# Performance work log

Hardware: AMD Instinct MI355X
Metric: run time of the kernel (lower is better)

## Reference

```python
import jax, jax.numpy as jnp
import numpy as np
from jax import lax

N_EXPERTS = 8
TOP_K_EXPERTS = 2
N_PRIMITIVES = 16
TOP_K_PRIM = 4
RANK = 64
D_MODEL = 512
D_FF = 2048
BATCH, SEQ = 8, 2048
TEMPERATURE = 1.0
EPS = 1e-8


def setup_inputs() -> dict:
    key = jax.random.key(0)
    ks = jax.random.split(key, 8)
    x = jax.random.normal(ks[0], (BATCH, SEQ, D_MODEL), dtype=jnp.float32)
    Wr = jax.random.normal(ks[1], (N_EXPERTS, D_MODEL), dtype=jnp.float32) * 0.02
    fc1_logits = jax.random.normal(ks[2], (N_EXPERTS, N_PRIMITIVES), dtype=jnp.float32)
    fc2_logits = jax.random.normal(ks[3], (N_EXPERTS, N_PRIMITIVES), dtype=jnp.float32)
    A1 = jax.random.normal(ks[4], (N_PRIMITIVES, D_MODEL, RANK), dtype=jnp.float32) * 0.02
    B1 = jax.random.normal(ks[5], (N_PRIMITIVES, RANK, D_FF), dtype=jnp.float32) * 0.02
    A2 = jax.random.normal(ks[6], (N_PRIMITIVES, D_FF, RANK), dtype=jnp.float32) * 0.02
    B2 = jax.random.normal(ks[7], (N_PRIMITIVES, RANK, D_MODEL), dtype=jnp.float32) * 0.02
    return {"x": x, "Wr": Wr, "fc1_logits": fc1_logits, "fc2_logits": fc2_logits,
            "A1": A1, "B1": B1, "A2": A2, "B2": B2}


def _compose_fused(logits, A, B):
    """Build per-expert fused low-rank maps from primitive bank.
    logits: (E, P); A: (P, d_in, r); B: (P, r, d_out).
    Returns A_cat (E, d_in, k*r), B_cat (E, k*r, d_out)."""
    w = jax.nn.softmax(logits / TEMPERATURE, axis=-1)            # (E, P)
    top_w, top_idx = lax.top_k(w, TOP_K_PRIM)                     # (E, k)
    top_w = top_w / (top_w.sum(axis=-1, keepdims=True) + EPS)
    sqrt_w = jnp.sqrt(top_w + EPS)                                # (E, k)
    A_sel = A[top_idx] * sqrt_w[:, :, None, None]                 # (E, k, d_in, r)
    B_sel = B[top_idx] * sqrt_w[:, :, None, None]                 # (E, k, r, d_out)
    E = logits.shape[0]
    A_cat = jnp.transpose(A_sel, (0, 2, 1, 3)).reshape(E, A.shape[1], TOP_K_PRIM * RANK)
    B_cat = B_sel.reshape(E, TOP_K_PRIM * RANK, B.shape[2])
    return A_cat, B_cat


def reference(x, Wr, fc1_logits, fc2_logits, A1, B1, A2, B2):
    Bsz, S, D = x.shape
    T = Bsz * S
    xt = x.reshape(T, D)

    # --- router: top-k expert selection ---
    router_logits = xt @ Wr.T                                     # (T, E)
    router_probs = jax.nn.softmax(router_logits, axis=-1)         # (T, E)
    top_w, top_idx = lax.top_k(router_probs, TOP_K_EXPERTS)       # (T, K)
    top_w = top_w / (top_w.sum(axis=-1, keepdims=True) + EPS)
    rows = jnp.arange(T)[:, None]
    gate = jnp.zeros((T, N_EXPERTS), x.dtype).at[rows, top_idx].add(top_w)
    expert_mask = jnp.zeros((T, N_EXPERTS), x.dtype).at[rows, top_idx].set(1.0)

    # --- load balancing aux loss (Switch Transformer) ---
    tokens_per_expert = expert_mask.sum(axis=0)
    f = tokens_per_expert / (tokens_per_expert.sum() + EPS)
    P = router_probs.mean(axis=0)
    aux_loss = N_EXPERTS * jnp.sum(f * P)

    # --- per-expert composed FFN over shared primitive banks ---
    A1c, B1c = _compose_fused(fc1_logits, A1, B1)                 # (E, D, kr), (E, kr, Dff)
    A2c, B2c = _compose_fused(fc2_logits, A2, B2)                 # (E, Dff, kr), (E, kr, D)

    out = jnp.zeros((T, D), x.dtype)
    for e in range(N_EXPERTS):  # small fixed expert loop keeps peak memory at one expert's d_ff activation
        h = jax.nn.gelu((xt @ A1c[e]) @ B1c[e], approximate=False)  # (T, Dff)
        y = (h @ A2c[e]) @ B2c[e]                                   # (T, D)
        out = out + gate[:, e:e + 1] * y

    return out.reshape(Bsz, S, D), aux_loss
```

## Files before the change

kernel.cpp:

```cpp
#include <hip/hip_runtime.h>

#define T_TOK 16384
#define DM    512
#define DFF   2048
#define NE    8
#define NP    16
#define KP    4
#define RANK  64
#define KR    256
#define EPSF  1e-8f
#define CAP   6144
#define MT_E  48

typedef unsigned short u16;
typedef __bf16 bf16x8 __attribute__((ext_vector_type(8)));
typedef float  f32x4  __attribute__((ext_vector_type(4)));
typedef unsigned short u16x8v __attribute__((ext_vector_type(8)));
typedef unsigned short u16x4v __attribute__((ext_vector_type(4)));

typedef __attribute__((address_space(3))) void as3_void;
typedef __attribute__((address_space(1))) void as1_void;

__device__ __forceinline__ u16 f2bf(float f) {
  return __builtin_bit_cast(u16, (__bf16)f);
}
__device__ __forceinline__ float bf2f(u16 v) {
  unsigned int u = ((unsigned int)v) << 16;
  return __builtin_bit_cast(float, u);
}

__device__ __forceinline__ void gl_lds16(const u16* g, u16* l) {
  __builtin_amdgcn_global_load_lds((as1_void*)g, (as3_void*)l, 16, 0, 0);
}


__device__ __forceinline__ void stage_tile(const u16* g, int ld, u16* lds_tile, int tid) {
  int row = tid >> 3, cc = tid & 7;
#pragma unroll
  for (int ri = 0; ri < 4; ri++) {
    int rg = ri * 32 + row;
    gl_lds16(g + (size_t)rg * ld + ((cc ^ (rg & 7)) * 8), &lds_tile[rg * 64 + cc * 8]);
  }
}

__global__ void zero_kernel(int* __restrict__ cnt, float* __restrict__ probsum) {
  int i = blockIdx.x * 256 + threadIdx.x;
  if (i < NE) cnt[i] = 0;
  if (i >= NE && i < NE + NE * 64) probsum[i - NE] = 0.f;
}

__global__ void compose_meta(const float* __restrict__ fc1, const float* __restrict__ fc2,
                             float* __restrict__ sw1, int* __restrict__ idx1,
                             float* __restrict__ sw2, int* __restrict__ idx2) {
  int tid = threadIdx.x;
  if (tid >= 16) return;
  const float* src = (tid < 8) ? fc1 : fc2;
  float* sw = (tid < 8) ? sw1 : sw2;
  int*  idx = (tid < 8) ? idx1 : idx2;
  int e = tid & 7;
  float wv[NP];
  float mx = -1e30f;
  for (int p = 0; p < NP; p++) { wv[p] = src[e * NP + p]; mx = fmaxf(mx, wv[p]); }
  float sum = 0.f;
  for (int p = 0; p < NP; p++) { wv[p] = __expf(wv[p] - mx); sum += wv[p]; }
  float inv = 1.f / sum;
  for (int p = 0; p < NP; p++) wv[p] *= inv;
  float tw[KP]; int ti[KP];
  for (int k = 0; k < KP; k++) {
    int best = 0; float bv = -1.f;
    for (int p = 0; p < NP; p++) if (wv[p] > bv) { bv = wv[p]; best = p; }
    tw[k] = bv; ti[k] = best; wv[best] = -2.f;
  }
  float ts = tw[0] + tw[1] + tw[2] + tw[3];
  float invt = 1.f / (ts + EPSF);
  for (int k = 0; k < KP; k++) {
    sw[e * KP + k] = sqrtf(tw[k] * invt + EPSF);
    idx[e * KP + k] = ti[k];
  }
}

__global__ __launch_bounds__(256) void build_W1p(
    const float* __restrict__ A1, const int* __restrict__ idx1,
    const float* __restrict__ sw1, u16* __restrict__ W1p) {
  __shared__ u16 Ta[2 * 64 * 68];
  int bid = blockIdx.x;
  int k0i = bid & 7, ntile = (bid >> 3) & 1, e = bid >> 4;
  int d0 = k0i * 64;
  int tid = threadIdx.x;
  {
    int kk = tid >> 7, row = (tid >> 1) & 63, half = tid & 1;
    int prim = idx1[e * 4 + ntile * 2 + kk];
    float s = sw1[e * 4 + ntile * 2 + kk];
#pragma unroll
    for (int q = 0; q < 8; q++) {
      int r = half * 32 + q * 4;
      float4 v = *(const float4*)(A1 + ((size_t)prim * DM + d0 + row) * RANK + r);
      u16x4v o;
      o[0] = f2bf(v.x * s); o[1] = f2bf(v.y * s);
      o[2] = f2bf(v.z * s); o[3] = f2bf(v.w * s);
      *(u16x4v*)&Ta[(kk * 64 + row) * 68 + r] = o;
    }
  }
  __syncthreads();
  u16* dst = W1p + ((size_t)(e * 2 + ntile) * 8 + k0i) * 8192;
#pragma unroll
  for (int it = 0; it < 4; it++) {
    int slot = it * 256 + tid;
    int lane = slot & 63, rest = slot >> 6;
    int nt = rest & 3, ks = (rest >> 2) & 1, wn = rest >> 3;
    int ln = lane & 15, quad = lane >> 4;
    int r = nt * 16 + ln;
    int db = ks * 32 + quad * 8;
    u16x8v o;
#pragma unroll
    for (int j = 0; j < 8; j++) o[j] = Ta[(wn * 64 + db + j) * 68 + r];
    *(u16x8v*)&dst[((wn * 8 + ks * 4 + nt) * 64 + lane) * 8] = o;
  }
}

__global__ __launch_bounds__(256) void build_V1p(
    const float* __restrict__ B1, const int* __restrict__ idx1,
    const float* __restrict__ sw1, u16* __restrict__ V1p) {
  __shared__ u16 Tb[64 * 132];
  int bid = blockIdx.x;
  int p = bid & 3, f0i = (bid >> 2) & 15, e = bid >> 6;
  int prim = idx1[e * 4 + p];
  float s = sw1[e * 4 + p];
  int f0 = f0i * 128;
  int tid = threadIdx.x;
  {
    int r = tid >> 2, fq = (tid & 3) * 32;
#pragma unroll
    for (int q = 0; q < 8; q++) {
      int fl = fq + q * 4;
      float4 v = *(const float4*)(B1 + ((size_t)prim * RANK + r) * DFF + f0 + fl);
      u16x4v o;
      o[0] = f2bf(v.x * s); o[1] = f2bf(v.y * s);
      o[2] = f2bf(v.z * s); o[3] = f2bf(v.w * s);
      *(u16x4v*)&Tb[r * 132 + fl] = o;
    }
  }
  __syncthreads();
  u16* dst = V1p + ((size_t)e << 19) + f0i * 32768 + p * 8192;
#pragma unroll
  for (int it = 0; it < 4; it++) {
    int slot = it * 256 + tid;
    int lane = slot & 63, nt = (slot >> 6) & 1, ks = (slot >> 7) & 1, wv = slot >> 8;
    int ln = lane & 15, quad = lane >> 4;
    int fl = wv * 32 + nt * 16 + ln;
    int r0 = ks * 32 + quad * 8;
    u16x8v o;
#pragma unroll
    for (int j = 0; j < 8; j++) o[j] = Tb[(r0 + j) * 132 + fl];
    *(u16x8v*)&dst[(((wv * 2 + ks) * 2 + nt) * 64 + lane) * 8] = o;
  }
}

__global__ __launch_bounds__(256) void build_W2p(
    const float* __restrict__ A2, const int* __restrict__ idx2,
    const float* __restrict__ sw2, u16* __restrict__ W2p) {
  __shared__ u16 Ta[2 * 64 * 68];
  int bid = blockIdx.x;
  int c2 = bid & 3, f0i = (bid >> 2) & 15, e = bid >> 6;
  int hh = c2 >> 1, fi = c2 & 1;
  int f0 = f0i * 128 + fi * 64;
  int tid = threadIdx.x;
  {
    int kk = tid >> 7, row = (tid >> 1) & 63, half = tid & 1;
    int prim = idx2[e * 4 + hh * 2 + kk];
    float s = sw2[e * 4 + hh * 2 + kk];
#pragma unroll
    for (int q = 0; q < 8; q++) {
      int r = half * 32 + q * 4;
      float4 v = *(const float4*)(A2 + ((size_t)prim * DFF + f0 + row) * RANK + r);
      u16x4v o;
      o[0] = f2bf(v.x * s); o[1] = f2bf(v.y * s);
      o[2] = f2bf(v.z * s); o[3] = f2bf(v.w * s);
      *(u16x4v*)&Ta[(kk * 64 + row) * 68 + r] = o;
    }
  }
  __syncthreads();
  u16* dst = W2p + ((size_t)e << 19) + f0i * 32768 + c2 * 8192;
#pragma unroll
  for (int it = 0; it < 4; it++) {
    int slot = it * 256 + tid;
    int lane = slot & 63, nt = (slot >> 6) & 1, ks = (slot >> 7) & 1, wv = slot >> 8;
    int ln = lane & 15, quad = lane >> 4;
    int kk = wv >> 1;
    int r = (wv & 1) * 32 + nt * 16 + ln;
    int fb = ks * 32 + quad * 8;
    u16x8v o;
#pragma unroll
    for (int j = 0; j < 8; j++) o[j] = Ta[(kk * 64 + fb + j) * 68 + r];
    *(u16x8v*)&dst[(((wv * 2 + ks) * 2 + nt) * 64 + lane) * 8] = o;
  }
}

__global__ __launch_bounds__(256) void build_V2p(
    const float* __restrict__ B2, const int* __restrict__ idx2,
    const float* __restrict__ sw2, u16* __restrict__ V2p) {
  __shared__ u16 Tb[64 * 132];
  int bid = blockIdx.x;
  int k0i = bid & 3, ntile = (bid >> 2) & 3, e = bid >> 4;
  int prim = idx2[e * 4 + k0i];
  float s = sw2[e * 4 + k0i];
  int tid = threadIdx.x;
  {
    int r = tid >> 2, dq = (tid & 3) * 32;
#pragma unroll
    for (int q = 0; q < 8; q++) {
      int dd = dq + q * 4;
      float4 v = *(const float4*)(B2 + ((size_t)prim * RANK + r) * DM + ntile * 128 + dd);
      u16x4v o;
      o[0] = f2bf(v.x * s); o[1] = f2bf(v.y * s);
      o[2] = f2bf(v.z * s); o[3] = f2bf(v.w * s);
      *(u16x4v*)&Tb[r * 132 + dd] = o;
    }
  }
  __syncthreads();
  u16* dst = V2p + ((size_t)(e * 4 + ntile) * 4 + k0i) * 8192;
#pragma unroll
  for (int it = 0; it < 4; it++) {
    int slot = it * 256 + tid;
    int lane = slot & 63, rest = slot >> 6;
    int nt = rest & 3, ks = (rest >> 2) & 1, wn = rest >> 3;
    int ln = lane & 15, quad = lane >> 4;
    int dd = wn * 64 + nt * 16 + ln;
    int r0 = ks * 32 + quad * 8;
    u16x8v o;
#pragma unroll
    for (int j = 0; j < 8; j++) o[j] = Tb[(r0 + j) * 132 + dd];
    *(u16x8v*)&dst[((wn * 8 + ks * 4 + nt) * 64 + lane) * 8] = o;
  }
}

__global__ __launch_bounds__(256) void router_kernel(
    const float* __restrict__ x, const float* __restrict__ Wr,
    float* __restrict__ probsum, int* __restrict__ eidx,
    float* __restrict__ gate) {
  __shared__ float wr_s[NE * 4 * 132];
  __shared__ float ps_s[NE];
  int tid = threadIdx.x;
  if (tid < NE) ps_s[tid] = 0.f;
  for (int i = tid; i < NE * DM; i += 256) {
    int e = i >> 9, k = i & 511;
    wr_s[(e * 4 + (k >> 7)) * 132 + (k & 127)] = Wr[i];
  }
  __syncthreads();
  int lane = tid & 63, wv = tid >> 6;
  int tl = lane & 15, sl = lane >> 4;
  int t = blockIdx.x * 64 + wv * 16 + tl;
  const float* xp = x + (size_t)t * DM + sl * 128;
  const float* wp = &wr_s[sl * 132];
  float acc[NE];
#pragma unroll
  for (int e = 0; e < NE; e++) acc[e] = 0.f;
  for (int c = 0; c < 32; c++) {
    float4 xv = *(const float4*)(xp + c * 4);
#pragma unroll
    for (int e = 0; e < NE; e++) {
      float4 w4 = *(const float4*)(wp + e * 4 * 132 + c * 4);
      acc[e] += xv.x * w4.x + xv.y * w4.y + xv.z * w4.z + xv.w * w4.w;
    }
  }
#pragma unroll
  for (int e = 0; e < NE; e++) {
    acc[e] += __shfl_xor(acc[e], 16, 64);
    acc[e] += __shfl_xor(acc[e], 32, 64);
  }
  if (sl == 0) {
    float mx = acc[0];
#pragma unroll
    for (int e = 1; e < NE; e++) mx = fmaxf(mx, acc[e]);
    float pe[NE]; float sum = 0.f;
#pragma unroll
    for (int e = 0; e < NE; e++) { pe[e] = __expf(acc[e] - mx); sum += pe[e]; }
    float inv = 1.f / sum;
#pragma unroll
    for (int e = 0; e < NE; e++) pe[e] *= inv;
    int i0 = 0;
#pragma unroll
    for (int e = 1; e < NE; e++) if (pe[e] > pe[i0]) i0 = e;
    int i1 = (i0 == 0) ? 1 : 0;
#pragma unroll
    for (int e = 0; e < NE; e++) if (e != i0 && pe[e] > pe[i1]) i1 = e;
    float p0 = pe[i0], p1 = pe[i1];
    float gd = 1.f / (p0 + p1 + EPSF);
    eidx[t] = i0 | (i1 << 3);
    gate[i0 * T_TOK + t] = p0 * gd;
    gate[i1 * T_TOK + t] = p1 * gd;
#pragma unroll
    for (int e = 0; e < NE; e++) atomicAdd(&ps_s[e], pe[e]);
  }
  __syncthreads();
  if (tid < NE) atomicAdd(&probsum[tid * 64 + (blockIdx.x & 63)], ps_s[tid]);
}

__global__ void scatter_kernel(const int* __restrict__ eidx,
                               int* __restrict__ cnt, int* __restrict__ perm,
                               int* __restrict__ slots) {
  __shared__ int hist[NE], base[NE];
  int tid = threadIdx.x;
  if (tid < NE) hist[tid] = 0;
  __syncthreads();
  int t = blockIdx.x * 256 + tid;
  int pk = eidx[t];
  int e0 = pk & 7, e1 = (pk >> 3) & 7;
  int p0 = atomicAdd(&hist[e0], 1);
  int p1 = atomicAdd(&hist[e1], 1);
  __syncthreads();
  if (tid < NE) base[tid] = atomicAdd(&cnt[tid], hist[tid]);
  __syncthreads();
  int g0 = base[e0] + p0; if (g0 >= CAP) g0 = CAP - 1;
  int g1 = base[e1] + p1; if (g1 >= CAP) g1 = CAP - 1;
  perm[e0 * T_TOK + g0] = t;
  perm[e1 * T_TOK + g1] = t;
  slots[t * 2]     = e0 * CAP + g0;
  slots[t * 2 + 1] = e1 * CAP + g1;
}

__global__ void aux_kernel(const int* __restrict__ cnt, const float* __restrict__ probsum,
                           float* __restrict__ aux_out) {
  int lane = threadIdx.x;
  if (lane >= 64) return;
  float s[NE];
#pragma unroll
  for (int e = 0; e < NE; e++) {
    float v = probsum[e * 64 + lane];
#pragma unroll
    for (int off = 32; off > 0; off >>= 1) v += __shfl_xor(v, off, 64);
    s[e] = v;
  }
  if (lane == 0) {
    float c[NE]; float cs = 0.f;
    for (int e = 0; e < NE; e++) { c[e] = (float)cnt[e]; cs += c[e]; }
    float aux = 0.f;
    for (int e = 0; e < NE; e++)
      aux += (c[e] / (cs + EPSF)) * (s[e] / (float)T_TOK);
    *aux_out = (float)NE * aux;
  }
}


__global__ __launch_bounds__(256) void k1_u(
    const float* __restrict__ x, const int* __restrict__ cnt,
    const int* __restrict__ perm, const u16* __restrict__ W1p,
    u16* __restrict__ u) {
  __shared__ __align__(16) u16 As[8192];
  __shared__ int tok_s[128];
  int bid = blockIdx.x;
  int e = bid & 7;
  int r0 = bid >> 3;
  int ntile = r0 & 1, mt = r0 >> 1;
  int m0 = mt << 7;
  int cntE = cnt[e];
  if (m0 >= cntE) return;
  int tid = threadIdx.x;
  if (tid < 128) {
    int mm = m0 + tid; if (mm > cntE - 1) mm = cntE - 1;
    tok_s[tid] = perm[e * T_TOK + mm];
  }
  __syncthreads();
  int wv = tid >> 6, lane = tid & 63;
  int wm = wv >> 1, wn = wv & 1, ln = lane & 15, quad = lane >> 4;
  int sw = (ln & 7) << 3;
  const u16* Wbase = W1p + ((size_t)(e * 2 + ntile) * 8) * 8192 + (wn * 8 * 64 + lane) * 8;
  int kst = mt & 7;
  f32x4 acc[4][4];
#pragma unroll
  for (int a = 0; a < 4; a++)
#pragma unroll
    for (int b = 0; b < 4; b++) acc[a][b] = (f32x4){0.f, 0.f, 0.f, 0.f};
  for (int kk = 0; kk < 8; kk++) {
    int k0i = (kk + kst) & 7;
    bf16x8 bf[2][4];
    const u16* Wf = Wbase + (size_t)k0i * 8192;
#pragma unroll
    for (int ks = 0; ks < 2; ks++)
#pragma unroll
      for (int nt = 0; nt < 4; nt++)
        bf[ks][nt] = *(const bf16x8*)&Wf[(ks * 4 + nt) * 512];
    for (int i = tid; i < 2048; i += 256) {
      int row = i >> 4, c4 = i & 15;
      float4 v = *(const float4*)(x + (size_t)tok_s[row] * DM + k0i * 64 + c4 * 4);
      u16x4v o; o[0] = f2bf(v.x); o[1] = f2bf(v.y); o[2] = f2bf(v.z); o[3] = f2bf(v.w);
      *(u16x4v*)&As[row * 64 + ((c4 * 4) ^ ((row & 7) << 3))] = o;
    }
    __syncthreads();
#pragma unroll
    for (int ks = 0; ks < 2; ks++) {
      bf16x8 af[4];
      int co = (ks * 32 + quad * 8) ^ sw;
#pragma unroll
      for (int mt2 = 0; mt2 < 4; mt2++)
        af[mt2] = *(const bf16x8*)&As[(wm * 64 + mt2 * 16 + ln) * 64 + co];
      __builtin_amdgcn_s_setprio(1);
#pragma unroll
      for (int mt2 = 0; mt2 < 4; mt2++)
#pragma unroll
        for (int nt = 0; nt < 4; nt++)
          acc[mt2][nt] = __builtin_amdgcn_mfma_f32_16x16x32_bf16(af[mt2], bf[ks][nt], acc[mt2][nt], 0, 0, 0);
      __builtin_amdgcn_s_setprio(0);
    }
    __syncthreads();
  }
  int slot0 = e * CAP + m0;
#pragma unroll
  for (int mt2 = 0; mt2 < 4; mt2++)
#pragma unroll
    for (int nt = 0; nt < 4; nt++)
#pragma unroll
      for (int r = 0; r < 4; r++) {
        int row = wm * 64 + mt2 * 16 + quad * 4 + r;
        int col = ntile * 128 + wn * 64 + nt * 16 + ln;
        u[(size_t)(slot0 + row) * KR + col] = f2bf(acc[mt2][nt][r]);
      }
}

__global__ __launch_bounds__(256, 2) void k23(
    const u16* __restrict__ u, const int* __restrict__ cnt,
    const u16* __restrict__ V1p, const u16* __restrict__ W2p,
    u16* __restrict__ t) {
  __shared__ __align__(16) u16 Us16[64 * 128];
  __shared__ __align__(16) u16 Hs[64 * 128];
  int bid = blockIdx.x;
  int e = bid & 7, mt = bid >> 3;
  int m0 = mt << 6;
  int cntE = cnt[e];
  if (m0 >= cntE) return;
  int tid = threadIdx.x;
  int slot0 = e * CAP + m0;
  const u16* ub = u + (size_t)slot0 * KR;

#pragma unroll
  for (int r = 0; r < 4; r++) {
    int i = r * 256 + tid;
    int row = i >> 4, cc = i & 15;
    gl_lds16(ub + (size_t)row * 256 + 128 + ((cc ^ (row & 7)) * 8), &Us16[i * 8]);
  }

  int wv = tid >> 6, lane = tid & 63;
  int ln = lane & 15, quad = lane >> 4;
  int sw = (ln & 7) << 3;

  bf16x8 ureg[2][2][4];
#pragma unroll
  for (int p = 0; p < 2; p++)
#pragma unroll
    for (int ks = 0; ks < 2; ks++)
#pragma unroll
      for (int m = 0; m < 4; m++)
        ureg[p][ks][m] = *(const bf16x8*)&ub[(size_t)(m * 16 + ln) * KR + p * 64 + ks * 32 + quad * 8];

  __syncthreads();

  const u16* V1w = V1p + ((size_t)e << 19) + wv * 2048 + lane * 8;
  const u16* W2w = W2p + ((size_t)e << 19) + wv * 2048 + lane * 8;

  f32x4 tacc[4][4];
#pragma unroll
  for (int a = 0; a < 4; a++)
#pragma unroll
    for (int b = 0; b < 4; b++) tacc[a][b] = (f32x4){0.f, 0.f, 0.f, 0.f};
  f32x4 hacc[4][2];

  int fst = mt & 15;
  for (int ii = 0; ii < 16; ii++) {
    int f0i = (ii + fst) & 15;
    const u16* V1f = V1w + f0i * 32768;
    const u16* W2f = W2w + f0i * 32768;
#pragma unroll
    for (int p = 0; p < 4; p++) {
      bf16x8 bf[2][2];
#pragma unroll
      for (int ks = 0; ks < 2; ks++)
#pragma unroll
        for (int nt = 0; nt < 2; nt++)
          bf[ks][nt] = *(const bf16x8*)&V1f[p * 8192 + (ks * 2 + nt) * 512];
      if (p == 0) {
#pragma unroll
        for (int a = 0; a < 4; a++)
#pragma unroll
          for (int b = 0; b < 2; b++) hacc[a][b] = (f32x4){0.f, 0.f, 0.f, 0.f};
      }
      if (p < 2) {
        __builtin_amdgcn_s_setprio(1);
#pragma unroll
        for (int ks = 0; ks < 2; ks++)
#pragma unroll
          for (int m = 0; m < 4; m++)
#pragma unroll
            for (int nt = 0; nt < 2; nt++)
              hacc[m][nt] = __builtin_amdgcn_mfma_f32_16x16x32_bf16(ureg[p][ks][m], bf[ks][nt], hacc[m][nt], 0, 0, 0);
        __builtin_amdgcn_s_setprio(0);
      } else {
        bf16x8 af[2][4];
#pragma unroll
        for (int ks = 0; ks < 2; ks++) {
          int cu = ((p - 2) * 64 + ks * 32 + quad * 8) ^ sw;
#pragma unroll
          for (int m = 0; m < 4; m++)
            af[ks][m] = *(const bf16x8*)&Us16[((m * 16 + ln) << 7) + cu];
        }
        __builtin_amdgcn_s_setprio(1);
#pragma unroll
        for (int ks = 0; ks < 2; ks++)
#pragma unroll
          for (int m = 0; m < 4; m++)
#pragma unroll
            for (int nt = 0; nt < 2; nt++)
              hacc[m][nt] = __builtin_amdgcn_mfma_f32_16x16x32_bf16(af[ks][m], bf[ks][nt], hacc[m][nt], 0, 0, 0);
        __builtin_amdgcn_s_setprio(0);
      }
    }
    __syncthreads();
#pragma unroll
    for (int m = 0; m < 4; m++)
#pragma unroll
      for (int nt = 0; nt < 2; nt++)
#pragma unroll
        for (int r = 0; r < 4; r++) {
          int row = m * 16 + quad * 4 + r;
          int col = wv * 32 + nt * 16 + ln;
          float v = hacc[m][nt][r];
          float s = 1.f / (1.f + __expf(-1.702f * v));
          Hs[(row << 7) + (col ^ ((row & 7) << 3))] = f2bf(v * s);
        }
    __syncthreads();
#pragma unroll
    for (int c2 = 0; c2 < 4; c2++) {
      const int hh = c2 >> 1, fi = c2 & 1;
      bf16x8 bf[2][2], af[2][4];
#pragma unroll
      for (int ks = 0; ks < 2; ks++)
#pragma unroll
        for (int nt = 0; nt < 2; nt++)
          bf[ks][nt] = *(const bf16x8*)&W2f[c2 * 8192 + (ks * 2 + nt) * 512];
#pragma unroll
      for (int ks = 0; ks < 2; ks++) {
        int ch = (fi * 64 + ks * 32 + quad * 8) ^ sw;
#pragma unroll
        for (int m = 0; m < 4; m++)
          af[ks][m] = *(const bf16x8*)&Hs[((m * 16 + ln) << 7) + ch];
      }
      __builtin_amdgcn_s_setprio(1);
#pragma unroll
      for (int ks = 0; ks < 2; ks++)
#pragma unroll
        for (int m = 0; m < 4; m++)
#pragma unroll
          for (int nt = 0; nt < 2; nt++)
            tacc[m][hh * 2 + nt] = __builtin_amdgcn_mfma_f32_16x16x32_bf16(af[ks][m], bf[ks][nt], tacc[m][hh * 2 + nt], 0, 0, 0);
      __builtin_amdgcn_s_setprio(0);
    }
  }
#pragma unroll
  for (int m = 0; m < 4; m++)
#pragma unroll
    for (int hh = 0; hh < 2; hh++)
#pragma unroll
      for (int nt = 0; nt < 2; nt++)
#pragma unroll
        for (int r = 0; r < 4; r++) {
          int row = m * 16 + quad * 4 + r;
          int col = hh * 128 + wv * 32 + nt * 16 + ln;
          t[(size_t)(slot0 + row) * KR + col] = f2bf(tacc[m][hh * 2 + nt][r]);
        }
}

__global__ __launch_bounds__(256) void k4_y(
    const u16* __restrict__ t, const int* __restrict__ cnt,
    const int* __restrict__ perm, const float* __restrict__ gate,
    const u16* __restrict__ V2p, u16* __restrict__ y) {
  __shared__ __align__(16) u16 As[8192];
  __shared__ float g_s[128];
  int bid = blockIdx.x;
  int e = bid & 7;
  int r0 = bid >> 3;
  int ntile = r0 & 3, mt = r0 >> 2;
  int m0 = mt << 7;
  int cntE = cnt[e];
  if (m0 >= cntE) return;
  int tid = threadIdx.x;
  if (tid < 128) {
    int mm = m0 + tid; if (mm > cntE - 1) mm = cntE - 1;
    int tk = perm[e * T_TOK + mm];
    g_s[tid] = gate[e * T_TOK + tk];
  }
  __syncthreads();
  int slot0 = e * CAP + m0;
  const u16* Abase = t + (size_t)slot0 * KR;
  int wv = tid >> 6, lane = tid & 63;
  int wm = wv >> 1, wn = wv & 1, ln = lane & 15, quad = lane >> 4;
  int sw = (ln & 7) << 3;
  const u16* Wbase = V2p + ((size_t)(e * 4 + ntile) * 4) * 8192 + (wn * 8 * 64 + lane) * 8;
  int kst = mt & 3;
  f32x4 acc[4][4];
#pragma unroll
  for (int a = 0; a < 4; a++)
#pragma unroll
    for (int b = 0; b < 4; b++) acc[a][b] = (f32x4){0.f, 0.f, 0.f, 0.f};
  for (int kk = 0; kk < 4; kk++) {
    int k0i = (kk + kst) & 3;
    bf16x8 bf[2][4];
    const u16* Wf = Wbase + (size_t)k0i * 8192;
#pragma unroll
    for (int ks = 0; ks < 2; ks++)
#pragma unroll
      for (int nt = 0; nt < 4; nt++)
        bf[ks][nt] = *(const bf16x8*)&Wf[(ks * 4 + nt) * 512];
    stage_tile(Abase + k0i * 64, KR, As, tid);
    __syncthreads();
#pragma unroll
    for (int ks = 0; ks < 2; ks++) {
      bf16x8 af[4];
      int co = (ks * 32 + quad * 8) ^ sw;
#pragma unroll
      for (int mt2 = 0; mt2 < 4; mt2++)
        af[mt2] = *(const bf16x8*)&As[(wm * 64 + mt2 * 16 + ln) * 64 + co];
      __builtin_amdgcn_s_setprio(1);
#pragma unroll
      for (int mt2 = 0; mt2 < 4; mt2++)
#pragma unroll
        for (int nt = 0; nt < 4; nt++)
          acc[mt2][nt] = __builtin_amdgcn_mfma_f32_16x16x32_bf16(af[mt2], bf[ks][nt], acc[mt2][nt], 0, 0, 0);
      __builtin_amdgcn_s_setprio(0);
    }
    __syncthreads();
  }
#pragma unroll
  for (int mt2 = 0; mt2 < 4; mt2++)
#pragma unroll
    for (int nt = 0; nt < 4; nt++)
#pragma unroll
      for (int r = 0; r < 4; r++) {
        int row = wm * 64 + mt2 * 16 + quad * 4 + r;
        int col = ntile * 128 + wn * 64 + nt * 16 + ln;
        y[(size_t)(slot0 + row) * DM + col] = f2bf(acc[mt2][nt][r] * g_s[row]);
      }
}

__global__ void gather_kernel(const u16* __restrict__ y, const int* __restrict__ slots,
                              float* __restrict__ out) {
  int idx = blockIdx.x * 256 + threadIdx.x;
  int t = idx >> 7, c4 = (idx & 127) * 4;
  int sA = slots[t * 2], sB = slots[t * 2 + 1];
  u16x4v a = *(const u16x4v*)&y[(size_t)sA * DM + c4];
  u16x4v b = *(const u16x4v*)&y[(size_t)sB * DM + c4];
  float4 o;
  o.x = bf2f(a[0]) + bf2f(b[0]);
  o.y = bf2f(a[1]) + bf2f(b[1]);
  o.z = bf2f(a[2]) + bf2f(b[2]);
  o.w = bf2f(a[3]) + bf2f(b[3]);
  *(float4*)&out[(size_t)t * DM + c4] = o;
}

extern "C" void kernel_launch(void* const* d_in, const int* in_sizes, int n_in,
                              void* d_out, int out_size, void* d_ws, size_t ws_size,
                              hipStream_t stream) {
  const float* x   = (const float*)d_in[0];
  const float* Wr  = (const float*)d_in[1];
  const float* fc1 = (const float*)d_in[2];
  const float* fc2 = (const float*)d_in[3];
  const float* A1  = (const float*)d_in[4];
  const float* B1  = (const float*)d_in[5];
  const float* A2  = (const float*)d_in[6];
  const float* B2  = (const float*)d_in[7];
  float* out = (float*)d_out;

  char* ws = (char*)d_ws;
  float* sw1     = (float*)(ws + 0);
  int*   idx1    = (int*)(ws + 512);
  float* sw2     = (float*)(ws + 1024);
  int*   idx2    = (int*)(ws + 1536);
  int*   cnt     = (int*)(ws + 2048);
  float* probsum = (float*)(ws + 2560);
  int*   eidx    = (int*)(ws + 8192);
  int*   slots   = (int*)(ws + 8192 + 65536);
  float* gate    = (float*)(ws + 8192 + 65536 + 131072);
  int*   perm    = (int*)(ws + 8192 + 65536 + 131072 + 524288);
  u16*   W1p     = (u16*)(ws + 8192 + 65536 + 131072 + 2 * 524288);
  u16*   V1p     = W1p + 1048576;
  u16*   W2p     = V1p + 4194304;
  u16*   V2p     = W2p + 4194304;
  char*  endW    = (char*)(V2p + 1048576);
  u16*   u_buf   = (u16*)endW;
  u16*   t_buf   = (u16*)(endW + 25165824);
  u16*   y_buf   = (u16*)(endW + 2 * 25165824);

  zero_kernel<<<3, 256, 0, stream>>>(cnt, probsum);
  compose_meta<<<1, 64, 0, stream>>>(fc1, fc2, sw1, idx1, sw2, idx2);
  build_W1p<<<128, 256, 0, stream>>>(A1, idx1, sw1, W1p);
  build_V1p<<<512, 256, 0, stream>>>(B1, idx1, sw1, V1p);
  build_W2p<<<512, 256, 0, stream>>>(A2, idx2, sw2, W2p);
  build_V2p<<<128, 256, 0, stream>>>(B2, idx2, sw2, V2p);
  router_kernel<<<T_TOK / 64, 256, 0, stream>>>(x, Wr, probsum, eidx, gate);
  scatter_kernel<<<T_TOK / 256, 256, 0, stream>>>(eidx, cnt, perm, slots);
  aux_kernel<<<1, 64, 0, stream>>>(cnt, probsum, out + (out_size - 1));

  k1_u<<<2 * NE * MT_E, 256, 0, stream>>>(x, cnt, perm, W1p, u_buf);
  k23<<<NE * (CAP / 64), 256, 0, stream>>>(u_buf, cnt, V1p, W2p, t_buf);
  k4_y<<<4 * NE * MT_E, 256, 0, stream>>>(t_buf, cnt, perm, gate, V2p, y_buf);
  gather_kernel<<<T_TOK * DM / 4 / 256, 256, 0, stream>>>(y_buf, slots, out);
}
```

Baseline: 340.3 us.

## Double-buffer LDS tiles to drop trailing barriers and stagger start offsets

Shared-memory A tiles in k1_u and k4_y, and the H tile in k23, become ping-pong buffers. This lets each loop iteration drop its trailing __syncthreads, since the next stage writes into the other buffer. Start offsets for the K/F loops are spread with a multiply-by-5 rotation, and in k23 the order of the register and LDS phases plus the two output halves alternates by tile index. The aim is fewer barriers and less contention when blocks hit the same weight slices, at the cost of doubled LDS use, which may lower occupancy, and an unused empty lambda left in the code.

Result: slower. 490.6 us (+44.2%).

```diff
diff --git a/kernel.cpp b/kernel.cpp
--- a/kernel.cpp
+++ b/kernel.cpp
@@ -346,7 +346,7 @@
     const float* __restrict__ x, const int* __restrict__ cnt,
     const int* __restrict__ perm, const u16* __restrict__ W1p,
     u16* __restrict__ u) {
-  __shared__ __align__(16) u16 As[8192];
+  __shared__ __align__(16) u16 As[2][8192];
   __shared__ int tok_s[128];
   int bid = blockIdx.x;
   int e = bid & 7;
@@ -365,7 +365,7 @@
   int wm = wv >> 1, wn = wv & 1, ln = lane & 15, quad = lane >> 4;
   int sw = (ln & 7) << 3;
   const u16* Wbase = W1p + ((size_t)(e * 2 + ntile) * 8) * 8192 + (wn * 8 * 64 + lane) * 8;
-  int kst = mt & 7;
+  int kst = (mt * 5) & 7;
   f32x4 acc[4][4];
 #pragma unroll
   for (int a = 0; a < 4; a++)
@@ -373,6 +373,7 @@
     for (int b = 0; b < 4; b++) acc[a][b] = (f32x4){0.f, 0.f, 0.f, 0.f};
   for (int kk = 0; kk < 8; kk++) {
     int k0i = (kk + kst) & 7;
+    u16* Ac = As[kk & 1];
     bf16x8 bf[2][4];
     const u16* Wf = Wbase + (size_t)k0i * 8192;
 #pragma unroll
@@ -384,7 +385,7 @@
       int row = i >> 4, c4 = i & 15;
       float4 v = *(const float4*)(x + (size_t)tok_s[row] * DM + k0i * 64 + c4 * 4);
       u16x4v o; o[0] = f2bf(v.x); o[1] = f2bf(v.y); o[2] = f2bf(v.z); o[3] = f2bf(v.w);
-      *(u16x4v*)&As[row * 64 + ((c4 * 4) ^ ((row & 7) << 3))] = o;
+      *(u16x4v*)&Ac[row * 64 + ((c4 * 4) ^ ((row & 7) << 3))] = o;
     }
     __syncthreads();
 #pragma unroll
@@ -393,7 +394,7 @@
       int co = (ks * 32 + quad * 8) ^ sw;
 #pragma unroll
       for (int mt2 = 0; mt2 < 4; mt2++)
-        af[mt2] = *(const bf16x8*)&As[(wm * 64 + mt2 * 16 + ln) * 64 + co];
+        af[mt2] = *(const bf16x8*)&Ac[(wm * 64 + mt2 * 16 + ln) * 64 + co];
       __builtin_amdgcn_s_setprio(1);
 #pragma unroll
       for (int mt2 = 0; mt2 < 4; mt2++)
@@ -402,7 +403,6 @@
           acc[mt2][nt] = __builtin_amdgcn_mfma_f32_16x16x32_bf16(af[mt2], bf[ks][nt], acc[mt2][nt], 0, 0, 0);
       __builtin_amdgcn_s_setprio(0);
     }
-    __syncthreads();
   }
   int slot0 = e * CAP + m0;
 #pragma unroll
@@ -422,7 +422,7 @@
     const u16* __restrict__ V1p, const u16* __restrict__ W2p,
     u16* __restrict__ t) {
   __shared__ __align__(16) u16 Us16[64 * 128];
-  __shared__ __align__(16) u16 Hs[64 * 128];
+  __shared__ __align__(16) u16 Hs[2][64 * 128];
   int bid = blockIdx.x;
   int e = bid & 7, mt = bid >> 3;
   int m0 = mt << 6;
@@ -464,56 +464,71 @@
     for (int b = 0; b < 4; b++) tacc[a][b] = (f32x4){0.f, 0.f, 0.f, 0.f};
   f32x4 hacc[4][2];
 
-  int fst = mt & 15;
+  int fst  = (mt * 5) & 15;
+  int arot = (mt >> 4) & 1;
+  int brot = (mt >> 4) & 1;
+
+  auto phA_reg = [&](const u16* V1f) {
+#pragma unroll
+    for (int p = 0; p < 2; p++) {
+      bf16x8 bf[2][2];
+#pragma unroll
+      for (int ks = 0; ks < 2; ks++)
+#pragma unroll
+        for (int nt = 0; nt < 2; nt++)
+          bf[ks][nt] = *(const bf16x8*)&V1f[p * 8192 + (ks * 2 + nt) * 512];
+      __builtin_amdgcn_s_setprio(1);
+#pragma unroll
+      for (int ks = 0; ks < 2; ks++)
+#pragma unroll
+        for (int m = 0; m < 4; m++)
+#pragma unroll
+          for (int nt = 0; nt < 2; nt++)
+            hacc[m][nt] = __builtin_amdgcn_mfma_f32_16x16x32_bf16(ureg[p][ks][m], bf[ks][nt], hacc[m][nt], 0, 0, 0);
+      __builtin_amdgcn_s_setprio(0);
+    }
+  };
+  auto phA_lds = [&](const u16* V1f) {
+#pragma unroll
+    for (int p = 2; p < 4; p++) {
+      bf16x8 bf[2][2], af[2][4];
+#pragma unroll
+      for (int ks = 0; ks < 2; ks++)
+#pragma unroll
+        for (int nt = 0; nt < 2; nt++)
+          bf[ks][nt] = *(const bf16x8*)&V1f[p * 8192 + (ks * 2 + nt) * 512];
+#pragma unroll
+      for (int ks = 0; ks < 2; ks++) {
+        int cu = ((p - 2) * 64 + ks * 32 + quad * 8) ^ sw;
+#pragma unroll
+        for (int m = 0; m < 4; m++)
+          af[ks][m] = *(const bf16x8*)&Us16[((m * 16 + ln) << 7) + cu];
+      }
+      __builtin_amdgcn_s_setprio(1);
+#pragma unroll
+      for (int ks = 0; ks < 2; ks++)
+#pragma unroll
+        for (int m = 0; m < 4; m++)
+#pragma unroll
+          for (int nt = 0; nt < 2; nt++)
+            hacc[m][nt] = __builtin_amdgcn_mfma_f32_16x16x32_bf16(af[ks][m], bf[ks][nt], hacc[m][nt], 0, 0, 0);
+      __builtin_amdgcn_s_setprio(0);
+    }
+  };
+  auto phB = [&](const u16* W2f, const u16* Hc, int hh_c2base) {
+  };
+
   for (int ii = 0; ii < 16; ii++) {
     int f0i = (ii + fst) & 15;
     const u16* V1f = V1w + f0i * 32768;
     const u16* W2f = W2w + f0i * 32768;
-#pragma unroll
-    for (int p = 0; p < 4; p++) {
-      bf16x8 bf[2][2];
-#pragma unroll
-      for (int ks = 0; ks < 2; ks++)
-#pragma unroll
-        for (int nt = 0; nt < 2; nt++)
-          bf[ks][nt] = *(const bf16x8*)&V1f[p * 8192 + (ks * 2 + nt) * 512];
-      if (p == 0) {
-#pragma unroll
-        for (int a = 0; a < 4; a++)
-#pragma unroll
-          for (int b = 0; b < 2; b++) hacc[a][b] = (f32x4){0.f, 0.f, 0.f, 0.f};
-      }
-      if (p < 2) {
-        __builtin_amdgcn_s_setprio(1);
-#pragma unroll
-        for (int ks = 0; ks < 2; ks++)
-#pragma unroll
-          for (int m = 0; m < 4; m++)
-#pragma unroll
-            for (int nt = 0; nt < 2; nt++)
-              hacc[m][nt] = __builtin_amdgcn_mfma_f32_16x16x32_bf16(ureg[p][ks][m], bf[ks][nt], hacc[m][nt], 0, 0, 0);
-        __builtin_amdgcn_s_setprio(0);
-      } else {
-        bf16x8 af[2][4];
-#pragma unroll
-        for (int ks = 0; ks < 2; ks++) {
-          int cu = ((p - 2) * 64 + ks * 32 + quad * 8) ^ sw;
-#pragma unroll
-          for (int m = 0; m < 4; m++)
-            af[ks][m] = *(const bf16x8*)&Us16[((m * 16 + ln) << 7) + cu];
-        }
-        __builtin_amdgcn_s_setprio(1);
-#pragma unroll
-        for (int ks = 0; ks < 2; ks++)
-#pragma unroll
-          for (int m = 0; m < 4; m++)
-#pragma unroll
-            for (int nt = 0; nt < 2; nt++)
-              hacc[m][nt] = __builtin_amdgcn_mfma_f32_16x16x32_bf16(af[ks][m], bf[ks][nt], hacc[m][nt], 0, 0, 0);
-        __builtin_amdgcn_s_setprio(0);
-      }
-    }
-    __syncthreads();
+    u16* Hc = Hs[ii & 1];
+#pragma unroll
+    for (int a = 0; a < 4; a++)
+#pragma unroll
+      for (int b = 0; b < 2; b++) hacc[a][b] = (f32x4){0.f, 0.f, 0.f, 0.f};
+    if (arot) { phA_lds(V1f); phA_reg(V1f); }
+    else      { phA_reg(V1f); phA_lds(V1f); }
 #pragma unroll
     for (int m = 0; m < 4; m++)
 #pragma unroll
@@ -524,36 +539,67 @@
           int col = wv * 32 + nt * 16 + ln;
           float v = hacc[m][nt][r];
           float s = 1.f / (1.f + __expf(-1.702f * v));
-          Hs[(row << 7) + (col ^ ((row & 7) << 3))] = f2bf(v * s);
+          Hc[(row << 7) + (col ^ ((row & 7) << 3))] = f2bf(v * s);
         }
     __syncthreads();
 #pragma unroll
-    for (int c2 = 0; c2 < 4; c2++) {
-      const int hh = c2 >> 1, fi = c2 & 1;
-      bf16x8 bf[2][2], af[2][4];
-#pragma unroll
-      for (int ks = 0; ks < 2; ks++)
-#pragma unroll
-        for (int nt = 0; nt < 2; nt++)
-          bf[ks][nt] = *(const bf16x8*)&W2f[c2 * 8192 + (ks * 2 + nt) * 512];
-#pragma unroll
-      for (int ks = 0; ks < 2; ks++) {
-        int ch = (fi * 64 + ks * 32 + quad * 8) ^ sw;
-#pragma unroll
-        for (int m = 0; m < 4; m++)
-          af[ks][m] = *(const bf16x8*)&Hs[((m * 16 + ln) << 7) + ch];
+    for (int half = 0; half < 2; half++) {
+      if ((half == 0) != (brot != 0)) {
+#pragma unroll
+        for (int fi = 0; fi < 2; fi++) {
+          bf16x8 bf[2][2], af[2][4];
+#pragma unroll
+          for (int ks = 0; ks < 2; ks++)
+#pragma unroll
+            for (int nt = 0; nt < 2; nt++)
+              bf[ks][nt] = *(const bf16x8*)&W2f[(0 * 2 + fi) * 8192 + (ks * 2 + nt) * 512];
+#pragma unroll
+          for (int ks = 0; ks < 2; ks++) {
+            int ch = (fi * 64 + ks * 32 + quad * 8) ^ sw;
+#pragma unroll
+            for (int m = 0; m < 4; m++)
+              af[ks][m] = *(const bf16x8*)&Hc[((m * 16 + ln) << 7) + ch];
+          }
+          __builtin_amdgcn_s_setprio(1);
+#pragma unroll
+          for (int ks = 0; ks < 2; ks++)
+#pragma unroll
+            for (int m = 0; m < 4; m++)
+#pragma unroll
+              for (int nt = 0; nt < 2; nt++)
+                tacc[m][0 * 2 + nt] = __builtin_amdgcn_mfma_f32_16x16x32_bf16(af[ks][m], bf[ks][nt], tacc[m][0 * 2 + nt], 0, 0, 0);
+          __builtin_amdgcn_s_setprio(0);
+        }
+      } else {
+#pragma unroll
+        for (int fi = 0; fi < 2; fi++) {
+          bf16x8 bf[2][2], af[2][4];
+#pragma unroll
+          for (int ks = 0; ks < 2; ks++)
+#pragma unroll
+            for (int nt = 0; nt < 2; nt++)
+              bf[ks][nt] = *(const bf16x8*)&W2f[(1 * 2 + fi) * 8192 + (ks * 2 + nt) * 512];
+#pragma unroll
+          for (int ks = 0; ks < 2; ks++) {
+            int ch = (fi * 64 + ks * 32 + quad * 8) ^ sw;
+#pragma unroll
+            for (int m = 0; m < 4; m++)
+              af[ks][m] = *(const bf16x8*)&Hc[((m * 16 + ln) << 7) + ch];
+          }
+          __builtin_amdgcn_s_setprio(1);
+#pragma unroll
+          for (int ks = 0; ks < 2; ks++)
+#pragma unroll
+            for (int m = 0; m < 4; m++)
+#pragma unroll
+              for (int nt = 0; nt < 2; nt++)
+                tacc[m][1 * 2 + nt] = __builtin_amdgcn_mfma_f32_16x16x32_bf16(af[ks][m], bf[ks][nt], tacc[m][1 * 2 + nt], 0, 0, 0);
+          __builtin_amdgcn_s_setprio(0);
+        }
       }
-      __builtin_amdgcn_s_setprio(1);
-#pragma unroll
-      for (int ks = 0; ks < 2; ks++)
-#pragma unroll
-        for (int m = 0; m < 4; m++)
-#pragma unroll
-          for (int nt = 0; nt < 2; nt++)
-            tacc[m][hh * 2 + nt] = __builtin_amdgcn_mfma_f32_16x16x32_bf16(af[ks][m], bf[ks][nt], tacc[m][hh * 2 + nt], 0, 0, 0);
-      __builtin_amdgcn_s_setprio(0);
-    }
-  }
+    }
+  }
+  (void)phB;
 #pragma unroll
   for (int m = 0; m < 4; m++)
 #pragma unroll
@@ -572,7 +618,7 @@
     const u16* __restrict__ t, const int* __restrict__ cnt,
     const int* __restrict__ perm, const float* __restrict__ gate,
     const u16* __restrict__ V2p, u16* __restrict__ y) {
-  __shared__ __align__(16) u16 As[8192];
+  __shared__ __align__(16) u16 As[2][8192];
   __shared__ float g_s[128];
   int bid = blockIdx.x;
   int e = bid & 7;
@@ -594,7 +640,7 @@
   int wm = wv >> 1, wn = wv & 1, ln = lane & 15, quad = lane >> 4;
   int sw = (ln & 7) << 3;
   const u16* Wbase = V2p + ((size_t)(e * 4 + ntile) * 4) * 8192 + (wn * 8 * 64 + lane) * 8;
-  int kst = mt & 3;
+  int kst = (mt * 5) & 3;
   f32x4 acc[4][4];
 #pragma unroll
   for (int a = 0; a < 4; a++)
@@ -602,6 +648,7 @@
     for (int b = 0; b < 4; b++) acc[a][b] = (f32x4){0.f, 0.f, 0.f, 0.f};
   for (int kk = 0; kk < 4; kk++) {
     int k0i = (kk + kst) & 3;
+    u16* Ac = As[kk & 1];
     bf16x8 bf[2][4];
     const u16* Wf = Wbase + (size_t)k0i * 8192;
 #pragma unroll
@@ -609,7 +656,7 @@
 #pragma unroll
       for (int nt = 0; nt < 4; nt++)
         bf[ks][nt] = *(const bf16x8*)&Wf[(ks * 4 + nt) * 512];
-    stage_tile(Abase + k0i * 64, KR, As, tid);
+    stage_tile(Abase + k0i * 64, KR, Ac, tid);
     __syncthreads();
 #pragma unroll
     for (int ks = 0; ks < 2; ks++) {
@@ -617,7 +664,7 @@
       int co = (ks * 32 + quad * 8) ^ sw;
 #pragma unroll
       for (int mt2 = 0; mt2 < 4; mt2++)
-        af[mt2] = *(const bf16x8*)&As[(wm * 64 + mt2 * 16 + ln) * 64 + co];
+        af[mt2] = *(const bf16x8*)&Ac[(wm * 64 + mt2 * 16 + ln) * 64 + co];
       __builtin_amdgcn_s_setprio(1);
 #pragma unroll
       for (int mt2 = 0; mt2 < 4; mt2++)
@@ -626,7 +673,6 @@
           acc[mt2][nt] = __builtin_amdgcn_mfma_f32_16x16x32_bf16(af[mt2], bf[ks][nt], acc[mt2][nt], 0, 0, 0);
       __builtin_amdgcn_s_setprio(0);
     }
-    __syncthreads();
   }
 #pragma unroll
   for (int mt2 = 0; mt2 < 4; mt2++)
```
